# Kernel optimization log

Hardware: AMD Instinct MI355X
Metric: run time of the kernel (lower is better)

## Reference

```python
import jax, jax.numpy as jnp
import numpy as np

B, S, D = 2, 2048, 2048
NH, NKV, HD = 16, 4, 128  # num_heads, num_key_value_heads, head_dim

def setup_inputs() -> dict:
    key = jax.random.key(0)
    ks = jax.random.split(key, 5)
    sc = 0.02
    return {
        "hidden_states": jax.random.normal(ks[0], (B, S, D), jnp.float32),
        "Wq": jax.random.normal(ks[1], (NH * HD, D), jnp.float32) * sc,
        "Wk": jax.random.normal(ks[2], (NKV * HD, D), jnp.float32) * sc,
        "Wv": jax.random.normal(ks[3], (NKV * HD, D), jnp.float32) * sc,
        "Wo": jax.random.normal(ks[4], (D, NH * HD), jnp.float32) * sc,
    }

def reference(hidden_states, Wq, Wk, Wv, Wo):
    b, s, d = hidden_states.shape
    # projections (LLaMA linear: x @ W.T)
    q = jnp.einsum('bsd,ed->bse', hidden_states, Wq).reshape(b, s, NH, HD).transpose(0, 2, 1, 3)
    k = jnp.einsum('bsd,ed->bse', hidden_states, Wk).reshape(b, s, NKV, HD).transpose(0, 2, 1, 3)
    v = jnp.einsum('bsd,ed->bse', hidden_states, Wv).reshape(b, s, NKV, HD).transpose(0, 2, 1, 3)
    # GQA: repeat kv heads
    n_rep = NH // NKV
    k = jnp.repeat(k, n_rep, axis=1)  # [b, NH, s, HD]
    v = jnp.repeat(v, n_rep, axis=1)
    scale = 1.0 / jnp.sqrt(jnp.asarray(HD, hidden_states.dtype))
    scores = jnp.einsum('bhqd,bhkd->bhqk', q, k) * scale
    causal = jnp.tril(jnp.ones((s, s), bool))
    scores = jnp.where(causal, scores, jnp.asarray(-jnp.inf, scores.dtype))
    attn = jax.nn.softmax(scores, axis=-1)
    out = jnp.einsum('bhqk,bhkd->bhqd', attn, v)  # [b, NH, s, HD]
    out = out.transpose(0, 2, 1, 3).reshape(b, s, NH * HD)
    return jnp.einsum('bse,de->bsd', out, Wo)
```

## Files before the change

### kernel.cpp

```cpp
#include <hip/hip_runtime.h>

typedef unsigned short u16;
typedef unsigned int u32;
typedef __attribute__((ext_vector_type(4))) float f32x4;
typedef __attribute__((ext_vector_type(16))) float f32x16;
typedef __attribute__((ext_vector_type(8))) short bf16x8;


__device__ __forceinline__ u16 f2b(float f) {
  u32 u = __builtin_bit_cast(u32, f);
  u = (u + 0x7fffu + ((u >> 16) & 1u)) >> 16;
  return (u16)u;
}

__device__ __forceinline__ void gload_lds16(const void* g, void* l) {
  __builtin_amdgcn_global_load_lds((const __attribute__((address_space(1))) u32*)g,
                                   (__attribute__((address_space(3))) u32*)l, 16, 0, 0);
}

#if __has_builtin(__builtin_amdgcn_permlane32_swap)
#define HAS_PLS 1
__device__ __forceinline__ void pls(u32 x, u32 y, u32& rx, u32& ry) {
  auto r = __builtin_amdgcn_permlane32_swap(x, y, false, false);
  rx = (u32)r[0];
  ry = (u32)r[1];
}
#endif

__device__ __forceinline__ float xhalf_max(float v) {
#ifdef HAS_PLS
  u32 a, b;
  pls(__builtin_bit_cast(u32, v), __builtin_bit_cast(u32, v), a, b);
  return fmaxf(__builtin_bit_cast(float, a), __builtin_bit_cast(float, b));
#else
  return fmaxf(v, __shfl_xor(v, 32));
#endif
}

__device__ __forceinline__ float xhalf_sum(float v) {
#ifdef HAS_PLS
  u32 a, b;
  pls(__builtin_bit_cast(u32, v), __builtin_bit_cast(u32, v), a, b);
  return __builtin_bit_cast(float, a) + __builtin_bit_cast(float, b);
#else
  return v + __shfl_xor(v, 32);
#endif
}

__device__ __forceinline__ void xexchange(int hi, u32 a0, u32 a1, u32 a2, u32 a3, u32* o) {
#ifdef HAS_PLS
  pls(a0, a2, o[0], o[2]);
  pls(a1, a3, o[1], o[3]);
#else
  u32 xa0 = (u32)__shfl_xor((int)a0, 32), xa1 = (u32)__shfl_xor((int)a1, 32);
  u32 xa2 = (u32)__shfl_xor((int)a2, 32), xa3 = (u32)__shfl_xor((int)a3, 32);
  o[0] = hi ? xa2 : a0;
  o[1] = hi ? xa3 : a1;
  o[2] = hi ? a2 : xa0;
  o[3] = hi ? a3 : xa1;
#endif
}

__device__ __forceinline__ u32 pktrunc(float lo, float hif) {
  return (__builtin_bit_cast(u32, lo) >> 16) | (__builtin_bit_cast(u32, hif) & 0xffff0000u);
}

__global__ void cvt_bf16(const float* __restrict__ src, u16* __restrict__ dst, int n) {
  int stride = gridDim.x * blockDim.x * 4;
  for (int idx = (blockIdx.x * blockDim.x + threadIdx.x) * 4; idx < n; idx += stride) {
    float4 v = *(const float4*)(src + idx);
    ushort4 o;
    o.x = f2b(v.x); o.y = f2b(v.y); o.z = f2b(v.z); o.w = f2b(v.w);
    *(ushort4*)(dst + idx) = o;
  }
}

__global__ void cvt_w4(const float* __restrict__ Wq, const float* __restrict__ Wk,
                       const float* __restrict__ Wv, const float* __restrict__ Wo,
                       u16* __restrict__ dst) {
  const int total = 10485760;
  int stride = gridDim.x * blockDim.x * 4;
  for (int idx = (blockIdx.x * blockDim.x + threadIdx.x) * 4; idx < total; idx += stride) {
    const float* src;
    int off;
    if (idx < 4194304) { src = Wq; off = idx; }
    else if (idx < 5242880) { src = Wk; off = idx - 4194304; }
    else if (idx < 6291456) { src = Wv; off = idx - 5242880; }
    else { src = Wo; off = idx - 6291456; }
    float4 v = *(const float4*)(src + off);
    ushort4 o;
    o.x = f2b(v.x); o.y = f2b(v.y); o.z = f2b(v.z); o.w = f2b(v.w);
    *(ushort4*)(dst + idx) = o;
  }
}

template<int OUT_MODE>
__global__ __launch_bounds__(512) void gemm256(const u16* __restrict__ A, const u16* __restrict__ B,
                                               void* __restrict__ Cout, int M, int N, int Kd,
                                               u16* __restrict__ Kout, u16* __restrict__ Vout) {
  __shared__ u16 smem[65536];
  const int tid = threadIdx.x;
  const int l = tid & 63, w = tid >> 6;
  const int c = l & 15, g = l >> 4;
  const int wr = w >> 2, wc = w & 3;
  const int tm = blockIdx.y * 256, tn = blockIdx.x * 256;

  const int lr = tid >> 3;
  const int lcol = (tid & 7) * 8;
  const int scol = lcol ^ (((lr >> 1) & 3) << 4);
  const int swc = ((c >> 1) & 3) << 4;

#define BARX() do { __builtin_amdgcn_s_barrier(); asm volatile("" ::: "memory"); } while (0)
#define STG(SRC, GROW0, LDS0) \
  gload_lds16((SRC) + (size_t)((GROW0) + lr) * Kd + k0n + scol, (LDS0) + lr * 64 + lcol)

  f32x4 acc[8][4] = {};

  {
    const int k0n = 0;
    u16* sAn = smem;
    u16* sBn = smem + 16384;
    STG(B, tn + 0, sBn); STG(B, tn + 64, sBn + 64 * 64);
    STG(B, tn + 128, sBn + 128 * 64); STG(B, tn + 192, sBn + 192 * 64);
    STG(A, tm + 0, sAn); STG(A, tm + 128, sAn + 128 * 64);
    STG(A, tm + 64, sAn + 64 * 64); STG(A, tm + 192, sAn + 192 * 64);
  }

  const int nt = Kd >> 6;
  for (int t = 0; t < nt; ++t) {
    const int slot = t & 1;
    u16* sAc = smem + slot * 32768;
    u16* sBc = sAc + 16384;
    u16* sAn = smem + (slot ^ 1) * 32768;
    u16* sBn = sAn + 16384;
    const int k0n = (t + 1) << 6;
    const bool st = (t + 1) < nt;

    bf16x8 bfr[4][2], af[2][2];

#define APH(q)                                                                  \
  do {                                                                          \
    _Pragma("unroll") for (int m2 = 0; m2 < 2; ++m2)                            \
    _Pragma("unroll") for (int kk = 0; kk < 2; ++kk)                            \
        af[m2][kk] = *(const bf16x8*)(sAc + (wr * 128 + (q) * 32 + m2 * 16 + c) * 64 + \
                                      ((kk * 32 + g * 8) ^ swc));               \
    __builtin_amdgcn_s_setprio(1);                                              \
    _Pragma("unroll") for (int m2 = 0; m2 < 2; ++m2)                            \
    _Pragma("unroll") for (int n = 0; n < 4; ++n)                               \
    _Pragma("unroll") for (int kk = 0; kk < 2; ++kk)                            \
        acc[(q) * 2 + m2][n] = __builtin_amdgcn_mfma_f32_16x16x32_bf16(         \
            af[m2][kk], bfr[n][kk], acc[(q) * 2 + m2][n], 0, 0, 0);             \
    __builtin_amdgcn_s_setprio(0);                                              \
  } while (0)

    BARX();
    if (st) { STG(B, tn + 0, sBn); STG(B, tn + 64, sBn + 64 * 64); }
    if (st) asm volatile("s_waitcnt vmcnt(4)" ::: "memory");
    else    asm volatile("s_waitcnt vmcnt(2)" ::: "memory");
    BARX();
#pragma unroll
    for (int n = 0; n < 4; ++n)
#pragma unroll
      for (int kk = 0; kk < 2; ++kk)
        bfr[n][kk] = *(const bf16x8*)(sBc + (wc * 64 + n * 16 + c) * 64 +
                                      ((kk * 32 + g * 8) ^ swc));
    APH(0);
    if (st) { STG(B, tn + 128, sBn + 128 * 64); STG(B, tn + 192, sBn + 192 * 64); }
    APH(1);
    if (st) { STG(A, tm + 0, sAn); STG(A, tm + 128, sAn + 128 * 64); }
    if (st) asm volatile("s_waitcnt vmcnt(6)" ::: "memory");
    else    asm volatile("s_waitcnt vmcnt(0)" ::: "memory");
    BARX();
    APH(2);
    if (st) { STG(A, tm + 64, sAn + 64 * 64); STG(A, tm + 192, sAn + 192 * 64); }
    APH(3);
#undef APH
  }

  if constexpr (OUT_MODE == 3) {
    if (tn >= 2048) {
      const bool isK = tn < 2560;
      BARX();
#pragma unroll
      for (int mi = 0; mi < 8; ++mi)
#pragma unroll
        for (int n = 0; n < 4; ++n)
#pragma unroll
          for (int i = 0; i < 4; ++i) {
            int s = wr * 128 + (mi >> 1) * 32 + (mi & 1) * 16 + g * 4 + i;
            int e = wc * 64 + n * 16 + c;
            int chunk = (e >> 7) * 8 + (s >> 5);
            int off;
            if (isK) {
              int k = e & 127;
              off = chunk * 4096 + (k >> 4) * 512 + ((k >> 3) & 1) * 256 + (s & 31) * 8 + (k & 7);
            } else {
              int d = e & 127;
              off = chunk * 4096 + (((s >> 4) & 1) * 4 + (d >> 5)) * 512 + ((s >> 3) & 1) * 256 +
                    (d & 31) * 8 + (s & 7);
            }
            smem[off] = f2b(acc[mi][n][i]);
          }
      BARX();
      const int kvh_base = (tn - (isK ? 2048 : 2560)) >> 7;
      const int bb = tm >> 11;
      const int kvt0 = (tm & 2047) >> 5;
      u16* Out = isK ? Kout : Vout;
#pragma unroll
      for (int ch = 0; ch < 16; ++ch) {
        u16* dst = Out + (size_t)((bb * 4 + kvh_base + (ch >> 3)) * 64 + kvt0 + (ch & 7)) * 4096;
        *(bf16x8*)(dst + tid * 8) = *(const bf16x8*)(smem + ch * 4096 + tid * 8);
      }
      return;
    }
#pragma unroll
    for (int mi = 0; mi < 8; ++mi)
#pragma unroll
      for (int n = 0; n < 4; ++n)
#pragma unroll
        for (int i = 0; i < 4; ++i) {
          int row = tm + wr * 128 + (mi >> 1) * 32 + (mi & 1) * 16 + g * 4 + i;
          int col = tn + wc * 64 + n * 16 + c;
          ((u16*)Cout)[(size_t)row * 2048 + col] = f2b(acc[mi][n][i]);
        }
    return;
  }

#pragma unroll
  for (int mi = 0; mi < 8; ++mi)
#pragma unroll
    for (int n = 0; n < 4; ++n)
#pragma unroll
      for (int i = 0; i < 4; ++i) {
        int row = tm + wr * 128 + (mi >> 1) * 32 + (mi & 1) * 16 + g * 4 + i;
        int col = tn + wc * 64 + n * 16 + c;
        ((float*)Cout)[(size_t)row * N + col] = acc[mi][n][i];
      }
#undef STG
#undef BARX
}

__global__ __launch_bounds__(512) void gemm_op(const u16* __restrict__ A, const u16* __restrict__ B,
                                               float* __restrict__ Cout, int Kd) {
  __shared__ u16 smem[49152];
  const int tid = threadIdx.x;
  const int l = tid & 63, w = tid >> 6;
  const int c = l & 15, g = l >> 4;
  const int wr = w >> 2, wc = w & 3;
  const int tm = blockIdx.y * 256, tn = blockIdx.x * 128;

  const int lr = tid >> 3;
  const int lcol = (tid & 7) * 8;
  const int scol = lcol ^ (((lr >> 1) & 3) << 4);
  const int swc = ((c >> 1) & 3) << 4;

#define BARX() do { __builtin_amdgcn_s_barrier(); asm volatile("" ::: "memory"); } while (0)
#define STG(SRC, GROW0, LDS0) \
  gload_lds16((SRC) + (size_t)((GROW0) + lr) * Kd + k0n + scol, (LDS0) + lr * 64 + lcol)

  f32x4 acc[8][2] = {};

  {
    const int k0n = 0;
    u16* sAn = smem;
    u16* sBn = smem + 16384;
    STG(B, tn + 0, sBn); STG(B, tn + 64, sBn + 64 * 64);
    STG(A, tm + 0, sAn); STG(A, tm + 128, sAn + 128 * 64);
    STG(A, tm + 64, sAn + 64 * 64); STG(A, tm + 192, sAn + 192 * 64);
  }

  const int nt = Kd >> 6;
  for (int t = 0; t < nt; ++t) {
    const int slot = t & 1;
    u16* sAc = smem + slot * 24576;
    u16* sBc = sAc + 16384;
    u16* sAn = smem + (slot ^ 1) * 24576;
    u16* sBn = sAn + 16384;
    const int k0n = (t + 1) << 6;
    const bool st = (t + 1) < nt;

    bf16x8 bfr[2][2], af[2][2];

#define APH(q)                                                                  \
  do {                                                                          \
    _Pragma("unroll") for (int m2 = 0; m2 < 2; ++m2)                            \
    _Pragma("unroll") for (int kk = 0; kk < 2; ++kk)                            \
        af[m2][kk] = *(const bf16x8*)(sAc + (wr * 128 + (q) * 32 + m2 * 16 + c) * 64 + \
                                      ((kk * 32 + g * 8) ^ swc));               \
    __builtin_amdgcn_s_setprio(1);                                              \
    _Pragma("unroll") for (int m2 = 0; m2 < 2; ++m2)                            \
    _Pragma("unroll") for (int n = 0; n < 2; ++n)                               \
    _Pragma("unroll") for (int kk = 0; kk < 2; ++kk)                            \
        acc[(q) * 2 + m2][n] = __builtin_amdgcn_mfma_f32_16x16x32_bf16(         \
            af[m2][kk], bfr[n][kk], acc[(q) * 2 + m2][n], 0, 0, 0);             \
    __builtin_amdgcn_s_setprio(0);                                              \
  } while (0)

    BARX();
    if (st) { STG(B, tn + 0, sBn); STG(B, tn + 64, sBn + 64 * 64); }
    if (st) asm volatile("s_waitcnt vmcnt(4)" ::: "memory");
    else    asm volatile("s_waitcnt vmcnt(2)" ::: "memory");
    BARX();
#pragma unroll
    for (int n = 0; n < 2; ++n)
#pragma unroll
      for (int kk = 0; kk < 2; ++kk)
        bfr[n][kk] = *(const bf16x8*)(sBc + (wc * 32 + n * 16 + c) * 64 +
                                      ((kk * 32 + g * 8) ^ swc));
    APH(0);
    if (st) { STG(A, tm + 0, sAn); STG(A, tm + 128, sAn + 128 * 64); }
    APH(1);
    if (st) { STG(A, tm + 64, sAn + 64 * 64); STG(A, tm + 192, sAn + 192 * 64); }
    if (st) asm volatile("s_waitcnt vmcnt(6)" ::: "memory");
    else    asm volatile("s_waitcnt vmcnt(0)" ::: "memory");
    BARX();
    APH(2);
    APH(3);
#undef APH
  }

#pragma unroll
  for (int mi = 0; mi < 8; ++mi)
#pragma unroll
    for (int n = 0; n < 2; ++n)
#pragma unroll
      for (int i = 0; i < 4; ++i) {
        int row = tm + wr * 128 + (mi >> 1) * 32 + (mi & 1) * 16 + g * 4 + i;
        int col = tn + wc * 32 + n * 16 + c;
        Cout[(size_t)row * 2048 + col] = acc[mi][n][i];
      }
#undef STG
#undef BARX
}

__global__ __launch_bounds__(256, 2) void attn_fwd(const u16* __restrict__ Q, const u16* __restrict__ Kf,
                                                   const u16* __restrict__ Vf, u16* __restrict__ AO) {
  const int l = threadIdx.x & 63, w = threadIdx.x >> 6;
  const int ql = l & 31, hi = l >> 5;
  const int id = (int)blockIdx.x;
  const int xcd = id & 7, slot = id >> 3;
  const int bh = xcd + 8 * (slot >> 5);
  const int x = slot & 31;
  const int b = bh >> 4, h = bh & 15;
  const int kvh = h >> 2;

  __shared__ float4 mO[2][16][64];
  __shared__ float mML[2][2][64];

  const float sm = 0.08838834764831845f * 1.4426950408889634f;

  const u16* Kfb = Kf + (size_t)(b * 4 + kvh) * 64 * 4096 + l * 8;
  const u16* Vfb = Vf + (size_t)(b * 4 + kvh) * 64 * 4096 + l * 8;

#define LOADK(KF, KV0)                                                        \
  do {                                                                        \
    const u16* kb_ = Kfb + (size_t)((KV0) >> 5) * 4096;                       \
    _Pragma("unroll") for (int ck = 0; ck < 8; ++ck)                          \
        KF[ck] = *(const bf16x8*)(kb_ + ck * 512);                            \
  } while (0)

#define LOADV(VT, KV0)                                                        \
  do {                                                                        \
    const u16* vb_ = Vfb + (size_t)((KV0) >> 5) * 4096;                       \
    _Pragma("unroll") for (int ks = 0; ks < 2; ++ks)                          \
    _Pragma("unroll") for (int db = 0; db < 4; ++db)                          \
        VT[ks][db] = *(const bf16x8*)(vb_ + (ks * 4 + db) * 512);             \
  } while (0)

#define COMPUTE(KF, VT, KV0)                                                  \
  do {                                                                        \
    f32x16 sacc = {};                                                         \
    __builtin_amdgcn_s_setprio(1);                                            \
    _Pragma("unroll") for (int ck = 0; ck < 8; ++ck)                          \
        sacc = __builtin_amdgcn_mfma_f32_32x32x16_bf16(KF[ck], qf[ck], sacc, 0, 0, 0); \
    __builtin_amdgcn_s_setprio(0);                                            \
    if ((KV0) == q0) {                             \
      _Pragma("unroll") for (int r = 0; r < 16; ++r) {                        \
        int crow = (r & 3) + 8 * (r >> 2) + 4 * hi;                           \
        if (crow > ql) sacc[r] = -1e30f;                                      \
      }                                                                       \
    }                                                                         \
    float t0 = fmaxf(sacc[0], sacc[1]), t1 = fmaxf(sacc[2], sacc[3]);         \
    float t2 = fmaxf(sacc[4], sacc[5]), t3 = fmaxf(sacc[6], sacc[7]);         \
    float t4 = fmaxf(sacc[8], sacc[9]), t5 = fmaxf(sacc[10], sacc[11]);       \
    float t6 = fmaxf(sacc[12], sacc[13]), t7 = fmaxf(sacc[14], sacc[15]);     \
    float mx = fmaxf(fmaxf(fmaxf(t0, t1), fmaxf(t2, t3)),                     \
                     fmaxf(fmaxf(t4, t5), fmaxf(t6, t7)));                    \
    mx = xhalf_max(mx);                                                       \
    float p[16];                                                              \
    _Pragma("unroll") for (int r = 0; r < 16; ++r)                            \
        p[r] = exp2f((sacc[r] - mrow) * sm);                                  \
    if (!__all((mx - mrow) * sm <= 8.0f)) {                \
      float mnew = fmaxf(mrow, mx);                                           \
      float rs = exp2f((mrow - mnew) * sm);                                   \
      mrow = mnew;                                                            \
      lrow *= rs;                                                             \
      _Pragma("unroll") for (int db = 0; db < 4; ++db)                        \
      _Pragma("unroll") for (int r = 0; r < 16; ++r) acc[db][r] *= rs;        \
      _Pragma("unroll") for (int r = 0; r < 16; ++r)                          \
          p[r] = exp2f((sacc[r] - mrow) * sm);                                \
    }                                                                         \
    float s0 = p[0] + p[1], s1 = p[2] + p[3], s2 = p[4] + p[5], s3 = p[6] + p[7]; \
    float s4 = p[8] + p[9], s5 = p[10] + p[11], s6 = p[12] + p[13], s7 = p[14] + p[15]; \
    float psum = ((s0 + s1) + (s2 + s3)) + ((s4 + s5) + (s6 + s7));           \
    lrow += xhalf_sum(psum);                                                  \
    u32 a0 = pktrunc(p[0], p[1]), a1 = pktrunc(p[2], p[3]);                   \
    u32 a2 = pktrunc(p[4], p[5]), a3 = pktrunc(p[6], p[7]);                   \
    u32 b0 = pktrunc(p[8], p[9]), b1 = pktrunc(p[10], p[11]);                 \
    u32 b2 = pktrunc(p[12], p[13]), b3 = pktrunc(p[14], p[15]);               \
    union { bf16x8 v; u32 u[4]; } pa0, pa1;                                   \
    xexchange(hi, a0, a1, a2, a3, pa0.u);                                     \
    xexchange(hi, b0, b1, b2, b3, pa1.u);                                     \
    __builtin_amdgcn_s_setprio(1);                                            \
    _Pragma("unroll") for (int db = 0; db < 4; ++db) {                        \
      acc[db] = __builtin_amdgcn_mfma_f32_32x32x16_bf16(VT[0][db], pa0.v, acc[db], 0, 0, 0); \
      acc[db] = __builtin_amdgcn_mfma_f32_32x32x16_bf16(VT[1][db], pa1.v, acc[db], 0, 0, 0); \
    }                                                                         \
    __builtin_amdgcn_s_setprio(0);                                            \
  } while (0)

#define PUBLISH(SLOT)                                                         \
  do {                                                                        \
    _Pragma("unroll") for (int db = 0; db < 4; ++db)                          \
    _Pragma("unroll") for (int rq = 0; rq < 4; ++rq) {                        \
      float4 v;                                                               \
      v.x = acc[db][rq * 4 + 0];                                              \
      v.y = acc[db][rq * 4 + 1];                                              \
      v.z = acc[db][rq * 4 + 2];                                              \
      v.w = acc[db][rq * 4 + 3];                                              \
      mO[SLOT][db * 4 + rq][l] = v;                                           \
    }                                                                         \
    mML[SLOT][0][l] = mrow;                                                   \
    mML[SLOT][1][l] = lrow;                                                   \
  } while (0)

#define MERGE(SLOT)                                                           \
  do {                                                                        \
    float m1 = mML[SLOT][0][l], l1 = mML[SLOT][1][l];                         \
    float mnew = fmaxf(mrow, m1);                                             \
    float f0 = exp2f((mrow - mnew) * sm);                                     \
    float f1 = exp2f((m1 - mnew) * sm);                                       \
    mrow = mnew;                                                              \
    lrow = lrow * f0 + l1 * f1;                                               \
    _Pragma("unroll") for (int db = 0; db < 4; ++db)                          \
    _Pragma("unroll") for (int rq = 0; rq < 4; ++rq) {                        \
      float4 o1 = mO[SLOT][db * 4 + rq][l];                                   \
      acc[db][rq * 4 + 0] = acc[db][rq * 4 + 0] * f0 + o1.x * f1;             \
      acc[db][rq * 4 + 1] = acc[db][rq * 4 + 1] * f0 + o1.y * f1;             \
      acc[db][rq * 4 + 2] = acc[db][rq * 4 + 2] * f0 + o1.z * f1;             \
      acc[db][rq * 4 + 3] = acc[db][rq * 4 + 3] * f0 + o1.w * f1;             \
    }                                                                         \
  } while (0)

  for (int phase = 0; phase < 2; ++phase) {
    const int t = phase ? (63 - x) : x;
    const int q0 = t * 32;

    bf16x8 qf[8];
    {
      const u16* qb = Q + ((size_t)(b * 2048 + q0 + ql)) * 2048 + h * 128 + hi * 8;
#pragma unroll
      for (int ck = 0; ck < 8; ++ck) qf[ck] = *(const bf16x8*)(qb + ck * 16);
    }

    f32x16 acc[4] = {};
    float mrow = -1e30f, lrow = 0.f;

    bf16x8 kfa[8], kfb[8];
    bf16x8 vt[2][4];

    int kv0 = w * 32;
    if (kv0 <= q0) {
      LOADK(kfa, kv0);
      while (true) {
        LOADV(vt, kv0);
        bool more = kv0 + 128 <= q0;
        if (more) LOADK(kfb, kv0 + 128);
        COMPUTE(kfa, vt, kv0);
        if (!more) break;
        kv0 += 128;
        LOADV(vt, kv0);
        more = kv0 + 128 <= q0;
        if (more) LOADK(kfa, kv0 + 128);
        COMPUTE(kfb, vt, kv0);
        if (!more) break;
        kv0 += 128;
      }
    }

    if (w >= 2) PUBLISH(w - 2);
    __syncthreads();
    if (w < 2) MERGE(w);
    __syncthreads();
    if (w == 1) PUBLISH(0);
    __syncthreads();
    if (w == 0) {
      MERGE(0);
      float inv = 1.0f / lrow;
      u16* ob = AO + (size_t)(b * 2048 + q0 + ql) * 2048 + h * 128 + hi * 4;
#pragma unroll
      for (int db = 0; db < 4; ++db)
#pragma unroll
        for (int rq = 0; rq < 4; ++rq) {
          ushort4 o;
          o.x = f2b(acc[db][rq * 4 + 0] * inv);
          o.y = f2b(acc[db][rq * 4 + 1] * inv);
          o.z = f2b(acc[db][rq * 4 + 2] * inv);
          o.w = f2b(acc[db][rq * 4 + 3] * inv);
          *(ushort4*)(ob + db * 32 + rq * 8) = o;
        }
    }
    __syncthreads();
  }
#undef LOADK
#undef LOADV
#undef COMPUTE
#undef PUBLISH
#undef MERGE
}

extern "C" void kernel_launch(void* const* d_in, const int* in_sizes, int n_in,
                              void* d_out, int out_size, void* d_ws, size_t ws_size,
                              hipStream_t stream) {
  const float* X = (const float*)d_in[0];
  const float* Wq = (const float*)d_in[1];
  const float* Wk = (const float*)d_in[2];
  const float* Wv = (const float*)d_in[3];
  const float* Wo = (const float*)d_in[4];

  u16* ws = (u16*)d_ws;
  const size_t nX = 8388608;
  const size_t nWq = 4194304;
  const size_t nWk = 1048576;
  u16* Xb = ws;
  u16* Wqb = Xb + nX;
  u16* Wkb = Wqb + nWq;
  u16* Wvb = Wkb + nWk;
  u16* Wob = Wvb + nWk;
  u16* Qb = Wob + nWq;
  u16* Kfb = Qb + nX;
  u16* Vfb = Kfb + 2097152;
  u16* AOb = Vfb + 2097152;
  if (ws_size < (size_t)(39845888) * 2) return;

  cvt_bf16<<<2048, 256, 0, stream>>>(X, Xb, (int)nX);
  cvt_w4<<<2048, 256, 0, stream>>>(Wq, Wk, Wv, Wo, Wqb);

  gemm256<3><<<dim3(12, 16), 512, 0, stream>>>(Xb, Wqb, Qb, 4096, 3072, 2048, Kfb, Vfb);

  attn_fwd<<<dim3(1024), 256, 0, stream>>>(Qb, Kfb, Vfb, AOb);

  gemm_op<<<dim3(16, 16), 512, 0, stream>>>(AOb, Wob, (float*)d_out, 2048);
}
```

Measured before the change: 190.5 us.

## Fuse conversion kernels, overlap Wo conversion with QKV GEMM, software-pipeline QK MFMA

Merges the X and Wq/Wk/Wv bf16 conversions into one kernel. The Wo conversion moves into extra blocks of the QKV GEMM grid, so it runs alongside the GEMM tiles and uses otherwise idle CUs. The attention inner loop is split into a QK-MFMA stage and a softmax+PV stage, and the next tile's QK product is issued before the current tile's softmax so MFMA and VALU work can overlap. The cost is higher register pressure from the second score accumulator, plus a one-time launch count reduction.

```diff
diff --git a/kernel.cpp b/kernel.cpp
--- a/kernel.cpp
+++ b/kernel.cpp
@@ -65,28 +65,18 @@
   return (__builtin_bit_cast(u32, lo) >> 16) | (__builtin_bit_cast(u32, hif) & 0xffff0000u);
 }
 
-__global__ void cvt_bf16(const float* __restrict__ src, u16* __restrict__ dst, int n) {
-  int stride = gridDim.x * blockDim.x * 4;
-  for (int idx = (blockIdx.x * blockDim.x + threadIdx.x) * 4; idx < n; idx += stride) {
-    float4 v = *(const float4*)(src + idx);
-    ushort4 o;
-    o.x = f2b(v.x); o.y = f2b(v.y); o.z = f2b(v.z); o.w = f2b(v.w);
-    *(ushort4*)(dst + idx) = o;
-  }
-}
-
-__global__ void cvt_w4(const float* __restrict__ Wq, const float* __restrict__ Wk,
-                       const float* __restrict__ Wv, const float* __restrict__ Wo,
-                       u16* __restrict__ dst) {
-  const int total = 10485760;
+__global__ void cvt_all(const float* __restrict__ X, const float* __restrict__ Wq,
+                        const float* __restrict__ Wk, const float* __restrict__ Wv,
+                        u16* __restrict__ dst) {
+  const int total = 14680064;
   int stride = gridDim.x * blockDim.x * 4;
   for (int idx = (blockIdx.x * blockDim.x + threadIdx.x) * 4; idx < total; idx += stride) {
     const float* src;
     int off;
-    if (idx < 4194304) { src = Wq; off = idx; }
-    else if (idx < 5242880) { src = Wk; off = idx - 4194304; }
-    else if (idx < 6291456) { src = Wv; off = idx - 5242880; }
-    else { src = Wo; off = idx - 6291456; }
+    if (idx < 8388608) { src = X; off = idx; }
+    else if (idx < 12582912) { src = Wq; off = idx - 8388608; }
+    else if (idx < 13631488) { src = Wk; off = idx - 12582912; }
+    else { src = Wv; off = idx - 13631488; }
     float4 v = *(const float4*)(src + off);
     ushort4 o;
     o.x = f2b(v.x); o.y = f2b(v.y); o.z = f2b(v.z); o.w = f2b(v.w);
@@ -97,9 +87,27 @@
 template<int OUT_MODE>
 __global__ __launch_bounds__(512) void gemm256(const u16* __restrict__ A, const u16* __restrict__ B,
                                                void* __restrict__ Cout, int M, int N, int Kd,
-                                               u16* __restrict__ Kout, u16* __restrict__ Vout) {
+                                               u16* __restrict__ Kout, u16* __restrict__ Vout,
+                                               const float* __restrict__ WoSrc,
+                                               u16* __restrict__ WoDst) {
   __shared__ u16 smem[65536];
   const int tid = threadIdx.x;
+
+  if constexpr (OUT_MODE == 3) {
+    if (blockIdx.x >= 12) {
+      const int id = ((int)blockIdx.x - 12) * (int)gridDim.y + (int)blockIdx.y;
+      const int base = id * 65536;
+#pragma unroll 4
+      for (int j = tid * 4; j < 65536; j += 2048) {
+        float4 v = *(const float4*)(WoSrc + base + j);
+        ushort4 o;
+        o.x = f2b(v.x); o.y = f2b(v.y); o.z = f2b(v.z); o.w = f2b(v.w);
+        *(ushort4*)(WoDst + base + j) = o;
+      }
+      return;
+    }
+  }
+
   const int l = tid & 63, w = tid >> 6;
   const int c = l & 15, g = l >> 4;
   const int wr = w >> 2, wc = w & 3;
@@ -367,29 +375,33 @@
         VT[ks][db] = *(const bf16x8*)(vb_ + (ks * 4 + db) * 512);             \
   } while (0)
 
-#define COMPUTE(KF, VT, KV0)                                                  \
+#define QKC(SACC, KF)                                                         \
   do {                                                                        \
-    f32x16 sacc = {};                                                         \
+    SACC = (f32x16){};                                                        \
     __builtin_amdgcn_s_setprio(1);                                            \
     _Pragma("unroll") for (int ck = 0; ck < 8; ++ck)                          \
-        sacc = __builtin_amdgcn_mfma_f32_32x32x16_bf16(KF[ck], qf[ck], sacc, 0, 0, 0); \
+        SACC = __builtin_amdgcn_mfma_f32_32x32x16_bf16(KF[ck], qf[ck], SACC, 0, 0, 0); \
     __builtin_amdgcn_s_setprio(0);                                            \
+  } while (0)
+
+#define SMPV(SACC, VT, KV0)                                                   \
+  do {                                                                        \
     if ((KV0) == q0) {                             \
       _Pragma("unroll") for (int r = 0; r < 16; ++r) {                        \
         int crow = (r & 3) + 8 * (r >> 2) + 4 * hi;                           \
-        if (crow > ql) sacc[r] = -1e30f;                                      \
+        if (crow > ql) SACC[r] = -1e30f;                                      \
       }                                                                       \
     }                                                                         \
-    float t0 = fmaxf(sacc[0], sacc[1]), t1 = fmaxf(sacc[2], sacc[3]);         \
-    float t2 = fmaxf(sacc[4], sacc[5]), t3 = fmaxf(sacc[6], sacc[7]);         \
-    float t4 = fmaxf(sacc[8], sacc[9]), t5 = fmaxf(sacc[10], sacc[11]);       \
-    float t6 = fmaxf(sacc[12], sacc[13]), t7 = fmaxf(sacc[14], sacc[15]);     \
+    float t0 = fmaxf(SACC[0], SACC[1]), t1 = fmaxf(SACC[2], SACC[3]);         \
+    float t2 = fmaxf(SACC[4], SACC[5]), t3 = fmaxf(SACC[6], SACC[7]);         \
+    float t4 = fmaxf(SACC[8], SACC[9]), t5 = fmaxf(SACC[10], SACC[11]);       \
+    float t6 = fmaxf(SACC[12], SACC[13]), t7 = fmaxf(SACC[14], SACC[15]);     \
     float mx = fmaxf(fmaxf(fmaxf(t0, t1), fmaxf(t2, t3)),                     \
                      fmaxf(fmaxf(t4, t5), fmaxf(t6, t7)));                    \
     mx = xhalf_max(mx);                                                       \
     float p[16];                                                              \
     _Pragma("unroll") for (int r = 0; r < 16; ++r)                            \
-        p[r] = exp2f((sacc[r] - mrow) * sm);                                  \
+        p[r] = exp2f((SACC[r] - mrow) * sm);                                  \
     if (!__all((mx - mrow) * sm <= 8.0f)) {                \
       float mnew = fmaxf(mrow, mx);                                           \
       float rs = exp2f((mrow - mnew) * sm);                                   \
@@ -398,7 +410,7 @@
       _Pragma("unroll") for (int db = 0; db < 4; ++db)                        \
       _Pragma("unroll") for (int r = 0; r < 16; ++r) acc[db][r] *= rs;        \
       _Pragma("unroll") for (int r = 0; r < 16; ++r)                          \
-          p[r] = exp2f((sacc[r] - mrow) * sm);                                \
+          p[r] = exp2f((SACC[r] - mrow) * sm);                                \
     }                                                                         \
     float s0 = p[0] + p[1], s1 = p[2] + p[3], s2 = p[4] + p[5], s3 = p[6] + p[7]; \
     float s4 = p[8] + p[9], s5 = p[10] + p[11], s6 = p[12] + p[13], s7 = p[14] + p[15]; \
@@ -468,23 +480,35 @@
 
     bf16x8 kfa[8], kfb[8];
     bf16x8 vt[2][4];
+    f32x16 sacc_a, sacc_b;
 
     int kv0 = w * 32;
     if (kv0 <= q0) {
       LOADK(kfa, kv0);
+      bool more1 = kv0 + 128 <= q0;
+      if (more1) LOADK(kfb, kv0 + 128);
+      QKC(sacc_a, kfa);
       while (true) {
         LOADV(vt, kv0);
-        bool more = kv0 + 128 <= q0;
-        if (more) LOADK(kfb, kv0 + 128);
-        COMPUTE(kfa, vt, kv0);
-        if (!more) break;
-        kv0 += 128;
+        {
+          bool more2 = kv0 + 256 <= q0;
+          if (more2) LOADK(kfa, kv0 + 256);
+          if (more1) QKC(sacc_b, kfb);
+          SMPV(sacc_a, vt, kv0);
+          if (!more1) break;
+          kv0 += 128;
+          more1 = more2;
+        }
         LOADV(vt, kv0);
-        more = kv0 + 128 <= q0;
-        if (more) LOADK(kfa, kv0 + 128);
-        COMPUTE(kfb, vt, kv0);
-        if (!more) break;
-        kv0 += 128;
+        {
+          bool more2 = kv0 + 256 <= q0;
+          if (more2) LOADK(kfb, kv0 + 256);
+          if (more1) QKC(sacc_a, kfa);
+          SMPV(sacc_b, vt, kv0);
+          if (!more1) break;
+          kv0 += 128;
+          more1 = more2;
+        }
       }
     }
 
@@ -514,7 +538,8 @@
   }
 #undef LOADK
 #undef LOADV
-#undef COMPUTE
+#undef QKC
+#undef SMPV
 #undef PUBLISH
 #undef MERGE
 }
@@ -543,10 +568,10 @@
   u16* AOb = Vfb + 2097152;
   if (ws_size < (size_t)(39845888) * 2) return;
 
-  cvt_bf16<<<2048, 256, 0, stream>>>(X, Xb, (int)nX);
-  cvt_w4<<<2048, 256, 0, stream>>>(Wq, Wk, Wv, Wo, Wqb);
-
-  gemm256<3><<<dim3(12, 16), 512, 0, stream>>>(Xb, Wqb, Qb, 4096, 3072, 2048, Kfb, Vfb);
+  cvt_all<<<2048, 256, 0, stream>>>(X, Wq, Wk, Wv, Xb);
+
+  gemm256<3><<<dim3(16, 16), 512, 0, stream>>>(Xb, Wqb, Qb, 4096, 3072, 2048, Kfb, Vfb,
+                                               Wo, Wob);
 
   attn_fwd<<<dim3(1024), 256, 0, stream>>>(Qb, Kfb, Vfb, AOb);
 
```

Measured after the change: 512.8 us. +169.2%, slower.

## Merge input conversions and overlap Wo conversion with QKV GEMM

Applied to the files above, without the earlier changes.

Merges the separate X and Wq/Wk/Wv bf16 conversion kernels into one launch, which drops one kernel launch. Moves the Wo fp32-to-bf16 conversion into 64 extra blocks of the QKV GEMM grid. Those blocks convert a 64K-element slice each and exit, so the conversion fills the idle CUs left by the 192-block GEMM grid. The extra blocks take scheduler slots, and the work can finish at uneven times.

```diff
diff --git a/kernel.cpp b/kernel.cpp
--- a/kernel.cpp
+++ b/kernel.cpp
@@ -65,28 +65,18 @@
   return (__builtin_bit_cast(u32, lo) >> 16) | (__builtin_bit_cast(u32, hif) & 0xffff0000u);
 }
 
-__global__ void cvt_bf16(const float* __restrict__ src, u16* __restrict__ dst, int n) {
-  int stride = gridDim.x * blockDim.x * 4;
-  for (int idx = (blockIdx.x * blockDim.x + threadIdx.x) * 4; idx < n; idx += stride) {
-    float4 v = *(const float4*)(src + idx);
-    ushort4 o;
-    o.x = f2b(v.x); o.y = f2b(v.y); o.z = f2b(v.z); o.w = f2b(v.w);
-    *(ushort4*)(dst + idx) = o;
-  }
-}
-
-__global__ void cvt_w4(const float* __restrict__ Wq, const float* __restrict__ Wk,
-                       const float* __restrict__ Wv, const float* __restrict__ Wo,
-                       u16* __restrict__ dst) {
-  const int total = 10485760;
+__global__ void cvt_all(const float* __restrict__ X, const float* __restrict__ Wq,
+                        const float* __restrict__ Wk, const float* __restrict__ Wv,
+                        u16* __restrict__ dst) {
+  const int total = 14680064;
   int stride = gridDim.x * blockDim.x * 4;
   for (int idx = (blockIdx.x * blockDim.x + threadIdx.x) * 4; idx < total; idx += stride) {
     const float* src;
     int off;
-    if (idx < 4194304) { src = Wq; off = idx; }
-    else if (idx < 5242880) { src = Wk; off = idx - 4194304; }
-    else if (idx < 6291456) { src = Wv; off = idx - 5242880; }
-    else { src = Wo; off = idx - 6291456; }
+    if (idx < 8388608) { src = X; off = idx; }
+    else if (idx < 12582912) { src = Wq; off = idx - 8388608; }
+    else if (idx < 13631488) { src = Wk; off = idx - 12582912; }
+    else { src = Wv; off = idx - 13631488; }
     float4 v = *(const float4*)(src + off);
     ushort4 o;
     o.x = f2b(v.x); o.y = f2b(v.y); o.z = f2b(v.z); o.w = f2b(v.w);
@@ -97,9 +87,27 @@
 template<int OUT_MODE>
 __global__ __launch_bounds__(512) void gemm256(const u16* __restrict__ A, const u16* __restrict__ B,
                                                void* __restrict__ Cout, int M, int N, int Kd,
-                                               u16* __restrict__ Kout, u16* __restrict__ Vout) {
+                                               u16* __restrict__ Kout, u16* __restrict__ Vout,
+                                               const float* __restrict__ WoSrc,
+                                               u16* __restrict__ WoDst) {
   __shared__ u16 smem[65536];
   const int tid = threadIdx.x;
+
+  if constexpr (OUT_MODE == 3) {
+    if (blockIdx.x >= 12) {
+      const int id = ((int)blockIdx.x - 12) * (int)gridDim.y + (int)blockIdx.y;
+      const int base = id * 65536;
+#pragma unroll 4
+      for (int j = tid * 4; j < 65536; j += 2048) {
+        float4 v = *(const float4*)(WoSrc + base + j);
+        ushort4 o;
+        o.x = f2b(v.x); o.y = f2b(v.y); o.z = f2b(v.z); o.w = f2b(v.w);
+        *(ushort4*)(WoDst + base + j) = o;
+      }
+      return;
+    }
+  }
+
   const int l = tid & 63, w = tid >> 6;
   const int c = l & 15, g = l >> 4;
   const int wr = w >> 2, wc = w & 3;
@@ -543,10 +551,10 @@
   u16* AOb = Vfb + 2097152;
   if (ws_size < (size_t)(39845888) * 2) return;
 
-  cvt_bf16<<<2048, 256, 0, stream>>>(X, Xb, (int)nX);
-  cvt_w4<<<2048, 256, 0, stream>>>(Wq, Wk, Wv, Wo, Wqb);
-
-  gemm256<3><<<dim3(12, 16), 512, 0, stream>>>(Xb, Wqb, Qb, 4096, 3072, 2048, Kfb, Vfb);
+  cvt_all<<<2048, 256, 0, stream>>>(X, Wq, Wk, Wv, Xb);
+
+  gemm256<3><<<dim3(16, 16), 512, 0, stream>>>(Xb, Wqb, Qb, 4096, 3072, 2048, Kfb, Vfb,
+                                               Wo, Wob);
 
   attn_fwd<<<dim3(1024), 256, 0, stream>>>(Qb, Kfb, Vfb, AOb);
 
```

Measured after the change: 190.4 us. Within noise of the previous version (-0.1%).
